# Optimization experiments

Measured on AMD Instinct MI355X. Metric: run time of the kernel, lower is better.

Reference implementation:

```python
import jax, jax.numpy as jnp
import numpy as np

# graph constants
B, V, CG, K, H, IN = 4, 6250, 25000, 3, 64, 2
NUM_LIT = B * 2 * V          # 50_000 literal nodes
NUM_CLS = B * CG             # 100_000 clause nodes
E = K * NUM_CLS              # 300_000 (l2c, c2l) edge pairs
NUM_ROUND = 3
DEMON = float(np.sqrt(H))    # self.demon = sqrt(hidden_size)


def setup_inputs() -> dict:
    key = jax.random.key(0)
    ks = jax.random.split(key, 12)
    rng = np.random.default_rng(0)
    # each clause has K literal endpoints; edges stay inside their own graph
    cls_idx = np.repeat(np.arange(NUM_CLS), K)
    g = cls_idx // CG
    lit_idx = g * 2 * V + rng.integers(0, 2 * V, size=E)

    def lin(k, fi, fo):
        return (jax.random.normal(k, (fi, fo), jnp.float32) / np.sqrt(fi)).astype(jnp.float32)

    return {
        "feat_l2c": jax.random.normal(ks[0], (E, IN), jnp.float32),
        "feat_c2l": jax.random.normal(ks[1], (E, IN), jnp.float32),
        "lit_idx": jnp.asarray(lit_idx, jnp.int32),
        "cls_idx": jnp.asarray(cls_idx, jnp.int32),
        "W_l2c_init": lin(ks[2], IN, H), "b_l2c_init": jnp.zeros((H,), jnp.float32),
        "W_c2l_init": lin(ks[3], IN, H), "b_c2l_init": jnp.zeros((H,), jnp.float32),
        "msgl_W": (jax.random.normal(ks[4], (3, H, H), jnp.float32) / np.sqrt(H)).astype(jnp.float32),
        "msgl_b": jnp.zeros((3, H), jnp.float32),
        "merge_W0": lin(ks[5], 2 * H, H), "merge_b0": jnp.zeros((H,), jnp.float32),
        "merge_Wr": (jax.random.normal(ks[6], (2, H, H), jnp.float32) / np.sqrt(H)).astype(jnp.float32),
        "merge_br": jnp.zeros((2, H), jnp.float32),
        "msgc_W": (jax.random.normal(ks[7], (3, H, H), jnp.float32) / np.sqrt(H)).astype(jnp.float32),
        "msgc_b": jnp.zeros((3, H), jnp.float32),
        "ro_W": (jax.random.normal(ks[8], (2, H, H), jnp.float32) / np.sqrt(H)).astype(jnp.float32),
        "ro_b": jnp.zeros((2, H), jnp.float32),
        "ro_W2": lin(ks[9], H, 1), "ro_b2": jnp.zeros((1,), jnp.float32),
    }


def _mlp3(x, W, b):  # 3-layer MLP, ReLU between layers (num_fc = 3)
    x = jax.nn.relu(x @ W[0] + b[0])
    x = jax.nn.relu(x @ W[1] + b[1])
    return x @ W[2] + b[2]


def reference(feat_l2c, feat_c2l, lit_idx, cls_idx,
              W_l2c_init, b_l2c_init, W_c2l_init, b_c2l_init,
              msgl_W, msgl_b, merge_W0, merge_b0, merge_Wr, merge_br,
              msgc_W, msgc_b, ro_W, ro_b, ro_W2, ro_b2):
    # init edge embeddings (l2c_init / c2l_init linear layers)
    h_l2c = feat_l2c @ W_l2c_init + b_l2c_init   # [E, H]
    h_c2l = feat_c2l @ W_c2l_init + b_c2l_init   # [E, H]

    for _ in range(NUM_ROUND):
        # literal update: aggregate incoming c2l messages, exclude self edge (BP-style)
        agg_l = jax.ops.segment_sum(h_c2l, lit_idx, num_segments=NUM_LIT)   # [NUM_LIT, H]
        m = _mlp3((agg_l[lit_idx] - h_c2l) / DEMON, msgl_W, msgl_b)          # [E, H]
        x = jax.nn.relu(jnp.concatenate([m, h_l2c], axis=-1) @ merge_W0 + merge_b0)
        x = jax.nn.relu(x @ merge_Wr[0] + merge_br[0])
        h_l2c = x @ merge_Wr[1] + merge_br[1]                                # l2c_merge_update
        # clause update
        agg_c = jax.ops.segment_sum(h_l2c, cls_idx, num_segments=NUM_CLS)   # [NUM_CLS, H]
        h_c2l = _mlp3((agg_c[cls_idx] - h_l2c) / DEMON, msgc_W, msgc_b)

    # u_add_e_sum with zero node feats == scatter-add edge emb to dst;
    # literal nodes only receive c2l edges
    l_emb = jax.ops.segment_sum(h_c2l, lit_idx, num_segments=NUM_LIT)        # [NUM_LIT, H]
    # segment_reduce(num_variable*2, ..., 'mean') over per-graph literal blocks (uniform sizes)
    l_mean = l_emb.reshape(B, 2 * V, H).mean(axis=1)                          # [B, H]
    x = jax.nn.relu(l_mean @ ro_W[0] + ro_b[0])
    x = jax.nn.relu(x @ ro_W[1] + ro_b[1])
    return jax.nn.sigmoid(x @ ro_W2 + ro_b2).squeeze(-1)                      # [B]
```

## Files before the change

kernel.cpp:

```cpp
#include <hip/hip_runtime.h>
#include <hip/hip_bf16.h>
#include <stdint.h>

#define EDGES   300000
#define NLIT    50000
#define NGRAPH  4
#define EPG     75000
#define HDIM    64

#define OFF_HL2C   0
#define OFF_HC2L   38400000
#define OFF_AGG    76800000
#define OFF_WT     89600000
#define OFF_ROACC  89681920
#define OFF_CNT    89682944
#define OFF_CSROFF 89882944
#define OFF_CURSOR 90082948
#define OFF_EIDX   90282948
#define OFF_BSUM   91482948
#define OFF_BBASE  91484000

#define WT_TOTAL    40960
#define WT_CLS_ELEM 28672

#define LIT_WBYTES (7 * 8192)
#define CLS_WBYTES (3 * 8192)
#define EPB2       256
#define NCHUNK     ((EDGES + EPB2 - 1) / EPB2)
#define LIT_GRID   512
#define CLS_GRID   1024

#define SCAN_BLOCKS ((NLIT + 255) / 256)

typedef __attribute__((ext_vector_type(8)))  short          s16x8;
typedef __attribute__((ext_vector_type(8)))  unsigned short u16x8;
typedef __attribute__((ext_vector_type(4)))  unsigned short u16x4;
typedef __attribute__((ext_vector_type(4)))  float          f32x4;
typedef __attribute__((ext_vector_type(16))) float          f32x16;

__device__ __forceinline__ f32x16 mfma32(s16x8 a, s16x8 b, f32x16 c) {
    return __builtin_amdgcn_mfma_f32_32x32x16_bf16(a, b, c, 0, 0, 0);
}
__device__ __forceinline__ float bf2f(unsigned short s) {
    union { unsigned int u; float f; } v; v.u = ((unsigned int)s) << 16; return v.f;
}
__device__ __forceinline__ unsigned short f2bf(float f) {
    union { __hip_bfloat16 b; unsigned short s; } v;
    v.b = __float2bfloat16(f);
    return v.s;
}
__device__ __forceinline__ unsigned pk2(float a, float b) {
    return (unsigned)f2bf(a) | ((unsigned)f2bf(b) << 16);
}

__device__ __forceinline__ void layer32(const char* __restrict__ unitBase,
                                        const float* __restrict__ biasL,
                                        const s16x8 (&bin)[4], f32x16 (&acc)[2],
                                        int eL, int hi)
{
#pragma unroll
    for (int t = 0; t < 2; ++t)
#pragma unroll
        for (int g = 0; g < 4; ++g) {
            f32x4 bv = *(const f32x4*)(biasL + 32 * t + 8 * g + 4 * hi);
#pragma unroll
            for (int r = 0; r < 4; ++r) acc[t][4 * g + r] = bv[r];
        }
#pragma unroll
    for (int kb = 0; kb < 4; ++kb)
#pragma unroll
        for (int t = 0; t < 2; ++t) {
            int row = 32 * t + eL;
            s16x8 a = *(const s16x8*)(unitBase + row * 128 +
                                      ((32 * kb + 16 * hi) ^ ((row & 7) << 4)));
            acc[t] = mfma32(a, bin[kb], acc[t]);
        }
}

template<bool RELU>
__device__ __forceinline__ void relayout32(f32x16 (&acc)[2], s16x8 (&bout)[4],
                                           int bpidx, int hi)
{
    if (RELU) {
#pragma unroll
        for (int t = 0; t < 2; ++t)
#pragma unroll
            for (int i = 0; i < 16; ++i) acc[t][i] = fmaxf(acc[t][i], 0.f);
    }
#pragma unroll
    for (int kb = 0; kb < 4; ++kb) {
        int m0 = 2 * kb, m1 = 2 * kb + 1;
        int t0 = m0 >> 2, g0 = m0 & 3, t1 = m1 >> 2, g1 = m1 & 3;
        unsigned A0 = pk2(acc[t0][4 * g0 + 0], acc[t0][4 * g0 + 1]);
        unsigned A1 = pk2(acc[t0][4 * g0 + 2], acc[t0][4 * g0 + 3]);
        unsigned B0 = pk2(acc[t1][4 * g1 + 0], acc[t1][4 * g1 + 1]);
        unsigned B1 = pk2(acc[t1][4 * g1 + 2], acc[t1][4 * g1 + 3]);
        unsigned pA0 = (unsigned)__builtin_amdgcn_ds_bpermute(bpidx, (int)A0);
        unsigned pA1 = (unsigned)__builtin_amdgcn_ds_bpermute(bpidx, (int)A1);
        unsigned pB0 = (unsigned)__builtin_amdgcn_ds_bpermute(bpidx, (int)B0);
        unsigned pB1 = (unsigned)__builtin_amdgcn_ds_bpermute(bpidx, (int)B1);
        union { unsigned w[4]; s16x8 v; } u;
        u.w[0] = hi ? pB0 : A0;
        u.w[1] = hi ? pB1 : A1;
        u.w[2] = hi ? B0 : pA0;
        u.w[3] = hi ? B1 : pA1;
        bout[kb] = u.v;
    }
}

__device__ __forceinline__ void store32(const f32x16 (&acc)[2],
                                        unsigned short* __restrict__ dst, int hi)
{
#pragma unroll
    for (int t = 0; t < 2; ++t)
#pragma unroll
        for (int g = 0; g < 4; ++g) {
            u16x4 p;
#pragma unroll
            for (int r = 0; r < 4; ++r) p[r] = f2bf(acc[t][4 * g + r]);
            *(u16x4*)(dst + 32 * t + 8 * g + 4 * hi) = p;
        }
}

__global__ __launch_bounds__(256) void prep_weights(
    const float* __restrict__ msgl_W, const float* __restrict__ merge_W0,
    const float* __restrict__ merge_Wr, const float* __restrict__ msgc_W,
    unsigned short* __restrict__ wT)
{
    int gid = blockIdx.x * 256 + threadIdx.x;
    if (gid >= WT_TOTAL) return;
    int unit = gid >> 12;
    int o = (gid >> 6) & 63;
    int csw = gid & 63;
    int i = csw ^ ((o & 7) << 3);
    float v;
    if (unit < 3)       v = msgl_W[unit * 4096 + i * 64 + o];
    else if (unit < 5)  v = merge_W0[((unit - 3) * 64 + i) * 64 + o];
    else if (unit < 7)  v = merge_Wr[(unit - 5) * 4096 + i * 64 + o];
    else                v = msgc_W[(unit - 7) * 4096 + i * 64 + o];
    wT[gid] = f2bf(v);
}

__global__ __launch_bounds__(256) void csr_hist(const int* __restrict__ lit_idx,
                                                int* __restrict__ cnt)
{
    int e = blockIdx.x * 256 + threadIdx.x;
    if (e < EDGES) atomicAdd(&cnt[lit_idx[e]], 1);
}

__global__ __launch_bounds__(256) void scan1(const int* __restrict__ cnt,
                                             int* __restrict__ bsum)
{
    __shared__ int red[4];
    int i = blockIdx.x * 256 + threadIdx.x;
    int s = (i < NLIT) ? cnt[i] : 0;
#pragma unroll
    for (int off = 1; off < 64; off <<= 1) s += __shfl_xor(s, off, 64);
    if ((threadIdx.x & 63) == 0) red[threadIdx.x >> 6] = s;
    __syncthreads();
    if (threadIdx.x == 0) bsum[blockIdx.x] = red[0] + red[1] + red[2] + red[3];
}

__global__ __launch_bounds__(256) void scan2(const int* __restrict__ bsum,
                                             int* __restrict__ bbase)
{
    __shared__ int tmp[256];
    int t = threadIdx.x;
    int v = (t < SCAN_BLOCKS) ? bsum[t] : 0;
    tmp[t] = v;
    __syncthreads();
#pragma unroll
    for (int off = 1; off < 256; off <<= 1) {
        int add = (t >= off) ? tmp[t - off] : 0;
        __syncthreads();
        tmp[t] += add;
        __syncthreads();
    }
    if (t < SCAN_BLOCKS) bbase[t] = tmp[t] - v;
}

__global__ __launch_bounds__(256) void scan3(const int* __restrict__ cnt,
                                             const int* __restrict__ bbase,
                                             int* __restrict__ off,
                                             int* __restrict__ cursor)
{
    __shared__ int tmp[256];
    int t = threadIdx.x;
    int i = blockIdx.x * 256 + t;
    int v = (i < NLIT) ? cnt[i] : 0;
    tmp[t] = v;
    __syncthreads();
#pragma unroll
    for (int offs = 1; offs < 256; offs <<= 1) {
        int add = (t >= offs) ? tmp[t - offs] : 0;
        __syncthreads();
        tmp[t] += add;
        __syncthreads();
    }
    if (i < NLIT) {
        int ex = bbase[blockIdx.x] + tmp[t] - v;
        off[i] = ex; cursor[i] = ex;
    }
    if (i == NLIT - 1) off[NLIT] = EDGES;
}

__global__ __launch_bounds__(256) void csr_scatter(const int* __restrict__ lit_idx,
                                                   int* __restrict__ cursor,
                                                   int* __restrict__ eidx)
{
    int e = blockIdx.x * 256 + threadIdx.x;
    if (e >= EDGES) return;
    int pos = atomicAdd(&cursor[lit_idx[e]], 1);
    eidx[pos] = e;
}

__global__ __launch_bounds__(256) void aggregate(const unsigned short* __restrict__ h_c2l,
                                                 const int* __restrict__ off,
                                                 const int* __restrict__ eidx,
                                                 float* __restrict__ agg)
{
    int t = threadIdx.x;
    int lane8 = t & 7;
    int lit = blockIdx.x * 32 + (t >> 3);
    if (lit >= NLIT) return;
    int lo = off[lit], hi = off[lit + 1];
    float s[8] = {0, 0, 0, 0, 0, 0, 0, 0};
    for (int i = lo; i < hi; ++i) {
        int e = eidx[i];
        u16x8 hv = *(const u16x8*)(h_c2l + e * 64 + lane8 * 8);
#pragma unroll
        for (int j = 0; j < 8; ++j) s[j] += bf2f(hv[j]);
    }
    f32x4 a0, a1;
    a0[0] = s[0]; a0[1] = s[1]; a0[2] = s[2]; a0[3] = s[3];
    a1[0] = s[4]; a1[1] = s[5]; a1[2] = s[6]; a1[3] = s[7];
    *(f32x4*)(agg + lit * 64 + lane8 * 8)     = a0;
    *(f32x4*)(agg + lit * 64 + lane8 * 8 + 4) = a1;
}

__global__ __launch_bounds__(256) void init_kernel(
    const float* __restrict__ feat_l2c, const float* __restrict__ feat_c2l,
    const float* __restrict__ W_l2c, const float* __restrict__ b_l2c,
    const float* __restrict__ W_c2l, const float* __restrict__ b_c2l,
    unsigned short* __restrict__ h_l2c, unsigned short* __restrict__ h_c2l)
{
    int gid = blockIdx.x * 256 + threadIdx.x;
    if (gid >= EDGES * 8) return;
    int e = gid >> 3, fo = (gid & 7) << 3;
    float2 fl = *(const float2*)(feat_l2c + e * 2);
    float2 fc = *(const float2*)(feat_c2l + e * 2);

    u16x8 outl, outc;
#pragma unroll
    for (int j = 0; j < 8; ++j) {
        float wl0 = W_l2c[fo + j], wl1 = W_l2c[64 + fo + j];
        float wc0 = W_c2l[fo + j], wc1 = W_c2l[64 + fo + j];
        float vl = fl.x * wl0 + fl.y * wl1 + b_l2c[fo + j];
        float vc = fc.x * wc0 + fc.y * wc1 + b_c2l[fo + j];
        outl[j] = f2bf(vl);
        outc[j] = f2bf(vc);
    }
    *(u16x8*)(h_l2c + e * 64 + fo) = outl;
    *(u16x8*)(h_c2l + e * 64 + fo) = outc;
}

__global__ __launch_bounds__(512, 4) void lit_update(
    const unsigned short* __restrict__ h_c2l,
    unsigned short* __restrict__ h_l2c,
    const float* __restrict__ agg,
    const int* __restrict__ lit_idx,
    const unsigned short* __restrict__ wT,
    const float* __restrict__ msgl_b,
    const float* __restrict__ merge_b0,
    const float* __restrict__ merge_br)
{
    __shared__ __align__(16) char lds[LIT_WBYTES + 384 * 4];
    int tid = threadIdx.x;
#pragma unroll
    for (int c = 0; c < 7; ++c) {
        int idx = c * 512 + tid;
        *(u16x8*)(lds + idx * 16) = *(const u16x8*)(wT + idx * 8);
    }
    float* ldsBias = (float*)(lds + LIT_WBYTES);
    if (tid < 384) {
        float v;
        if (tid < 192)      v = msgl_b[tid];
        else if (tid < 256) v = merge_b0[tid - 192];
        else                v = merge_br[tid - 256];
        ldsBias[tid] = v;
    }
    __syncthreads();

    int wv = tid >> 6, lane = tid & 63;
    int eL = lane & 31, hi = lane >> 5;
    int bpidx = (lane ^ 32) << 2;

    for (int c = blockIdx.x; c < NCHUNK; c += LIT_GRID) {
        int base = c * EPB2 + wv * 32;
        if (base >= EDGES) continue;
        int e = base + eL;
        int lit = lit_idx[e];

        s16x8 hfrag[4];
#pragma unroll
        for (int k = 0; k < 4; ++k)
            hfrag[k] = *(const s16x8*)(h_l2c + e * 64 + 16 * k + 8 * hi);

        s16x8 binp[4];
#pragma unroll
        for (int k = 0; k < 4; ++k) {
            int f0 = 16 * k + 8 * hi;
            f32x4 a0 = *(const f32x4*)(agg + lit * 64 + f0);
            f32x4 a1 = *(const f32x4*)(agg + lit * 64 + f0 + 4);
            u16x8 hv = *(const u16x8*)(h_c2l + e * 64 + f0);
            s16x8 b;
#pragma unroll
            for (int j = 0; j < 4; ++j) b[j]     = (short)f2bf((a0[j] - bf2f(hv[j]))     * 0.125f);
#pragma unroll
            for (int j = 0; j < 4; ++j) b[4 + j] = (short)f2bf((a1[j] - bf2f(hv[4 + j])) * 0.125f);
            binp[k] = b;
        }

        f32x16 acc[2];
        s16x8 bf[4];
        layer32(lds,            ldsBias,       binp, acc, eL, hi);
        relayout32<true >(acc, bf, bpidx, hi);
        layer32(lds + 8192,     ldsBias + 64,  bf, acc, eL, hi);
        relayout32<true >(acc, bf, bpidx, hi);
        layer32(lds + 2 * 8192, ldsBias + 128, bf, acc, eL, hi);
        relayout32<false>(acc, bf, bpidx, hi);

#pragma unroll
        for (int t = 0; t < 2; ++t)
#pragma unroll
            for (int g = 0; g < 4; ++g) {
                f32x4 bv = *(const f32x4*)(ldsBias + 192 + 32 * t + 8 * g + 4 * hi);
#pragma unroll
                for (int r = 0; r < 4; ++r) acc[t][4 * g + r] = bv[r];
            }
#pragma unroll
        for (int kb = 0; kb < 8; ++kb) {
            const char* ub = lds + (3 + (kb >> 2)) * 8192;
            s16x8 bop = (kb < 4) ? bf[kb] : hfrag[kb - 4];
#pragma unroll
            for (int t = 0; t < 2; ++t) {
                int row = 32 * t + eL;
                s16x8 a = *(const s16x8*)(ub + row * 128 +
                                          ((32 * (kb & 3) + 16 * hi) ^ ((row & 7) << 4)));
                acc[t] = mfma32(a, bop, acc[t]);
            }
        }
        relayout32<true>(acc, bf, bpidx, hi);
        layer32(lds + 5 * 8192, ldsBias + 256, bf, acc, eL, hi);
        relayout32<true>(acc, bf, bpidx, hi);
        layer32(lds + 6 * 8192, ldsBias + 320, bf, acc, eL, hi);

        store32(acc, h_l2c + e * 64, hi);
    }
}

__global__ __launch_bounds__(512, 4) void clause_update(
    const unsigned short* __restrict__ h_l2c,
    unsigned short* __restrict__ h_c2l,
    const unsigned short* __restrict__ msgcT,
    const float* __restrict__ msgc_b)
{
    __shared__ __align__(16) char lds[CLS_WBYTES + 192 * 4];
    int tid = threadIdx.x;
#pragma unroll
    for (int c = 0; c < 3; ++c) {
        int idx = c * 512 + tid;
        *(u16x8*)(lds + idx * 16) = *(const u16x8*)(msgcT + idx * 8);
    }
    float* ldsBias = (float*)(lds + CLS_WBYTES);
    if (tid < 192) ldsBias[tid] = msgc_b[tid];
    __syncthreads();

    int wv = tid >> 6, lane = tid & 63;
    int eL = lane & 31, hi = lane >> 5;
    int bpidx = (lane ^ 32) << 2;

    for (int c = blockIdx.x; c < NCHUNK; c += CLS_GRID) {
        int base = c * EPB2 + wv * 32;
        if (base >= EDGES) continue;
        int e = base + eL;

        int c3 = (e / 3) * 3;
        int d = e - c3;
        int e1 = c3 + (d == 0 ? 1 : 0);
        int e2 = c3 + (d == 2 ? 1 : 2);

        s16x8 binp[4];
#pragma unroll
        for (int k = 0; k < 4; ++k) {
            int f0 = 16 * k + 8 * hi;
            u16x8 h1 = *(const u16x8*)(h_l2c + e1 * 64 + f0);
            u16x8 h2 = *(const u16x8*)(h_l2c + e2 * 64 + f0);
            s16x8 b;
#pragma unroll
            for (int j = 0; j < 8; ++j)
                b[j] = (short)f2bf((bf2f(h1[j]) + bf2f(h2[j])) * 0.125f);
            binp[k] = b;
        }

        f32x16 acc[2];
        s16x8 bf[4];
        layer32(lds,            ldsBias,       binp, acc, eL, hi);
        relayout32<true>(acc, bf, bpidx, hi);
        layer32(lds + 8192,     ldsBias + 64,  bf, acc, eL, hi);
        relayout32<true>(acc, bf, bpidx, hi);
        layer32(lds + 2 * 8192, ldsBias + 128, bf, acc, eL, hi);

        store32(acc, h_c2l + e * 64, hi);
    }
}

__global__ __launch_bounds__(256) void readout_sum(
    const unsigned short* __restrict__ h_c2l, float* __restrict__ ro_acc)
{
    __shared__ float lsum[32][64];
    int g = blockIdx.x >> 6, chunk = blockIdx.x & 63;
    int t = threadIdx.x;
    int fg = t & 7, el = t >> 3;
    float s[8] = {0, 0, 0, 0, 0, 0, 0, 0};
    for (int idx = chunk * 32 + el; idx < EPG; idx += 2048) {
        u16x8 hv = *(const u16x8*)(h_c2l + (g * EPG + idx) * 64 + fg * 8);
#pragma unroll
        for (int j = 0; j < 8; ++j) s[j] += bf2f(hv[j]);
    }
#pragma unroll
    for (int j = 0; j < 8; ++j) lsum[el][fg * 8 + j] = s[j];
    __syncthreads();
    if (t < 64) {
        float tot = 0.f;
#pragma unroll 8
        for (int r = 0; r < 32; ++r) tot += lsum[r][t];
        atomicAdd(&ro_acc[g * 64 + t], tot);
    }
}

__global__ __launch_bounds__(256) void readout_mlp(
    const float* __restrict__ ro_acc, const float* __restrict__ ro_W,
    const float* __restrict__ ro_b, const float* __restrict__ ro_W2,
    const float* __restrict__ ro_b2, float* __restrict__ out)
{
    __shared__ float xb[NGRAPH][HDIM];
    __shared__ float yb[NGRAPH][HDIM];
    int g = threadIdx.x >> 6;
    int j = threadIdx.x & 63;
    xb[g][j] = ro_acc[g * HDIM + j] * (1.0f / 12500.0f);
    __syncthreads();
    float a = ro_b[j];
#pragma unroll 8
    for (int k = 0; k < HDIM; ++k) a += xb[g][k] * ro_W[k * HDIM + j];
    a = fmaxf(a, 0.0f);
    yb[g][j] = a;
    __syncthreads();
    float a2 = ro_b[HDIM + j];
#pragma unroll 8
    for (int k = 0; k < HDIM; ++k) a2 += yb[g][k] * ro_W[4096 + k * HDIM + j];
    a2 = fmaxf(a2, 0.0f);
    float p = a2 * ro_W2[j];
#pragma unroll
    for (int off = 32; off > 0; off >>= 1) p += __shfl_down(p, off, 64);
    if (j == 0) out[g] = 1.0f / (1.0f + expf(-(p + ro_b2[0])));
}

extern "C" void kernel_launch(void* const* d_in, const int* in_sizes, int n_in,
                              void* d_out, int out_size, void* d_ws, size_t ws_size,
                              hipStream_t stream)
{
    const float* feat_l2c = (const float*)d_in[0];
    const float* feat_c2l = (const float*)d_in[1];
    const int*   lit_idx  = (const int*)d_in[2];
    const float* W_l2c    = (const float*)d_in[4];
    const float* b_l2c    = (const float*)d_in[5];
    const float* W_c2l    = (const float*)d_in[6];
    const float* b_c2l    = (const float*)d_in[7];
    const float* msgl_W   = (const float*)d_in[8];
    const float* msgl_b   = (const float*)d_in[9];
    const float* merge_W0 = (const float*)d_in[10];
    const float* merge_b0 = (const float*)d_in[11];
    const float* merge_Wr = (const float*)d_in[12];
    const float* merge_br = (const float*)d_in[13];
    const float* msgc_W   = (const float*)d_in[14];
    const float* msgc_b   = (const float*)d_in[15];
    const float* ro_W     = (const float*)d_in[16];
    const float* ro_b     = (const float*)d_in[17];
    const float* ro_W2    = (const float*)d_in[18];
    const float* ro_b2    = (const float*)d_in[19];

    char* ws = (char*)d_ws;
    unsigned short* h_l2c  = (unsigned short*)(ws + OFF_HL2C);
    unsigned short* h_c2l  = (unsigned short*)(ws + OFF_HC2L);
    float*          agg    = (float*)(ws + OFF_AGG);
    unsigned short* wT     = (unsigned short*)(ws + OFF_WT);
    float*          ro_acc = (float*)(ws + OFF_ROACC);
    int*            cnt    = (int*)(ws + OFF_CNT);
    int*            csroff = (int*)(ws + OFF_CSROFF);
    int*            cursor = (int*)(ws + OFF_CURSOR);
    int*            eidx   = (int*)(ws + OFF_EIDX);
    int*            bsum   = (int*)(ws + OFF_BSUM);
    int*            bbase  = (int*)(ws + OFF_BBASE);

    hipMemsetAsync(cnt, 0, NLIT * sizeof(int), stream);
    hipMemsetAsync(ro_acc, 0, NGRAPH * 64 * sizeof(float), stream);

    prep_weights<<<(WT_TOTAL + 255) / 256, 256, 0, stream>>>(msgl_W, merge_W0, merge_Wr, msgc_W, wT);

    csr_hist<<<(EDGES + 255) / 256, 256, 0, stream>>>(lit_idx, cnt);
    scan1<<<SCAN_BLOCKS, 256, 0, stream>>>(cnt, bsum);
    scan2<<<1, 256, 0, stream>>>(bsum, bbase);
    scan3<<<SCAN_BLOCKS, 256, 0, stream>>>(cnt, bbase, csroff, cursor);
    csr_scatter<<<(EDGES + 255) / 256, 256, 0, stream>>>(lit_idx, cursor, eidx);

    init_kernel<<<EDGES * 8 / 256, 256, 0, stream>>>(feat_l2c, feat_c2l, W_l2c, b_l2c,
                                                     W_c2l, b_c2l, h_l2c, h_c2l);
    for (int r = 0; r < 3; ++r) {
        aggregate<<<(NLIT + 31) / 32, 256, 0, stream>>>(h_c2l, csroff, eidx, agg);
        lit_update<<<LIT_GRID, 512, 0, stream>>>(h_c2l, h_l2c, agg, lit_idx, wT,
                                                 msgl_b, merge_b0, merge_br);
        clause_update<<<CLS_GRID, 512, 0, stream>>>(h_l2c, h_c2l, wT + WT_CLS_ELEM, msgc_b);
    }
    readout_sum<<<256, 256, 0, stream>>>(h_c2l, ro_acc);
    readout_mlp<<<1, 256, 0, stream>>>(ro_acc, ro_W, ro_b, ro_W2, ro_b2, (float*)d_out);
}
```

Before: 341.6 us.

## Fuse readout into final clause update, bf16 agg, unroll gather, one chunk per block

The final clause_update reduces its outputs per graph in-wave and accumulates them into ro_acc directly. This removes the last h_c2l store and the separate readout_sum pass. The aggregation buffer is now stored in bf16 to halve its traffic, and the gather loop is unrolled by four for more loads in flight. The edge kernels launch one block per 256-edge chunk instead of grid-striding, and the relayout uses two lane permutes instead of four. The bf16 aggregate adds rounding error to the sum before the subtraction, and the per-element shared atomics add reduction cost.

```diff
diff --git a/kernel.cpp b/kernel.cpp
--- a/kernel.cpp
+++ b/kernel.cpp
@@ -26,9 +26,7 @@
 #define LIT_WBYTES (7 * 8192)
 #define CLS_WBYTES (3 * 8192)
 #define EPB2       256
-#define NCHUNK     ((EDGES + EPB2 - 1) / EPB2)
-#define LIT_GRID   512
-#define CLS_GRID   1024
+#define GRID_EDGE  ((EDGES + EPB2 - 1) / EPB2)
 
 #define SCAN_BLOCKS ((NLIT + 255) / 256)
 
@@ -51,30 +49,6 @@
 }
 __device__ __forceinline__ unsigned pk2(float a, float b) {
     return (unsigned)f2bf(a) | ((unsigned)f2bf(b) << 16);
-}
-
-__device__ __forceinline__ void layer32(const char* __restrict__ unitBase,
-                                        const float* __restrict__ biasL,
-                                        const s16x8 (&bin)[4], f32x16 (&acc)[2],
-                                        int eL, int hi)
-{
-#pragma unroll
-    for (int t = 0; t < 2; ++t)
-#pragma unroll
-        for (int g = 0; g < 4; ++g) {
-            f32x4 bv = *(const f32x4*)(biasL + 32 * t + 8 * g + 4 * hi);
-#pragma unroll
-            for (int r = 0; r < 4; ++r) acc[t][4 * g + r] = bv[r];
-        }
-#pragma unroll
-    for (int kb = 0; kb < 4; ++kb)
-#pragma unroll
-        for (int t = 0; t < 2; ++t) {
-            int row = 32 * t + eL;
-            s16x8 a = *(const s16x8*)(unitBase + row * 128 +
-                                      ((32 * kb + 16 * hi) ^ ((row & 7) << 4)));
-            acc[t] = mfma32(a, bin[kb], acc[t]);
-        }
 }
 
 template<bool RELU>
@@ -95,15 +69,15 @@
         unsigned A1 = pk2(acc[t0][4 * g0 + 2], acc[t0][4 * g0 + 3]);
         unsigned B0 = pk2(acc[t1][4 * g1 + 0], acc[t1][4 * g1 + 1]);
         unsigned B1 = pk2(acc[t1][4 * g1 + 2], acc[t1][4 * g1 + 3]);
-        unsigned pA0 = (unsigned)__builtin_amdgcn_ds_bpermute(bpidx, (int)A0);
-        unsigned pA1 = (unsigned)__builtin_amdgcn_ds_bpermute(bpidx, (int)A1);
-        unsigned pB0 = (unsigned)__builtin_amdgcn_ds_bpermute(bpidx, (int)B0);
-        unsigned pB1 = (unsigned)__builtin_amdgcn_ds_bpermute(bpidx, (int)B1);
+        unsigned s0 = hi ? A0 : B0;
+        unsigned s1 = hi ? A1 : B1;
+        unsigned p0 = (unsigned)__builtin_amdgcn_ds_bpermute(bpidx, (int)s0);
+        unsigned p1 = (unsigned)__builtin_amdgcn_ds_bpermute(bpidx, (int)s1);
         union { unsigned w[4]; s16x8 v; } u;
-        u.w[0] = hi ? pB0 : A0;
-        u.w[1] = hi ? pB1 : A1;
-        u.w[2] = hi ? B0 : pA0;
-        u.w[3] = hi ? B1 : pA1;
+        u.w[0] = hi ? p0 : A0;
+        u.w[1] = hi ? p1 : A1;
+        u.w[2] = hi ? B0 : p0;
+        u.w[3] = hi ? B1 : p1;
         bout[kb] = u.v;
     }
 }
@@ -119,6 +93,30 @@
 #pragma unroll
             for (int r = 0; r < 4; ++r) p[r] = f2bf(acc[t][4 * g + r]);
             *(u16x4*)(dst + 32 * t + 8 * g + 4 * hi) = p;
+        }
+}
+
+__device__ __forceinline__ void layer32(const char* __restrict__ unitBase,
+                                        const float* __restrict__ biasL,
+                                        const s16x8 (&bin)[4], f32x16 (&acc)[2],
+                                        int eL, int hi)
+{
+#pragma unroll
+    for (int t = 0; t < 2; ++t)
+#pragma unroll
+        for (int g = 0; g < 4; ++g) {
+            f32x4 bv = *(const f32x4*)(biasL + 32 * t + 8 * g + 4 * hi);
+#pragma unroll
+            for (int r = 0; r < 4; ++r) acc[t][4 * g + r] = bv[r];
+        }
+#pragma unroll
+    for (int kb = 0; kb < 4; ++kb)
+#pragma unroll
+        for (int t = 0; t < 2; ++t) {
+            int row = 32 * t + eL;
+            s16x8 a = *(const s16x8*)(unitBase + row * 128 +
+                                      ((32 * kb + 16 * hi) ^ ((row & 7) << 4)));
+            acc[t] = mfma32(a, bin[kb], acc[t]);
         }
 }
 
@@ -217,7 +215,7 @@
 __global__ __launch_bounds__(256) void aggregate(const unsigned short* __restrict__ h_c2l,
                                                  const int* __restrict__ off,
                                                  const int* __restrict__ eidx,
-                                                 float* __restrict__ agg)
+                                                 unsigned short* __restrict__ agg)
 {
     int t = threadIdx.x;
     int lane8 = t & 7;
@@ -225,17 +223,27 @@
     if (lit >= NLIT) return;
     int lo = off[lit], hi = off[lit + 1];
     float s[8] = {0, 0, 0, 0, 0, 0, 0, 0};
-    for (int i = lo; i < hi; ++i) {
+    int i = lo;
+    for (; i + 4 <= hi; i += 4) {
+        int e0 = eidx[i], e1 = eidx[i + 1], e2 = eidx[i + 2], e3 = eidx[i + 3];
+        u16x8 v0 = *(const u16x8*)(h_c2l + e0 * 64 + lane8 * 8);
+        u16x8 v1 = *(const u16x8*)(h_c2l + e1 * 64 + lane8 * 8);
+        u16x8 v2 = *(const u16x8*)(h_c2l + e2 * 64 + lane8 * 8);
+        u16x8 v3 = *(const u16x8*)(h_c2l + e3 * 64 + lane8 * 8);
+#pragma unroll
+        for (int j = 0; j < 8; ++j)
+            s[j] += (bf2f(v0[j]) + bf2f(v1[j])) + (bf2f(v2[j]) + bf2f(v3[j]));
+    }
+    for (; i < hi; ++i) {
         int e = eidx[i];
         u16x8 hv = *(const u16x8*)(h_c2l + e * 64 + lane8 * 8);
 #pragma unroll
         for (int j = 0; j < 8; ++j) s[j] += bf2f(hv[j]);
     }
-    f32x4 a0, a1;
-    a0[0] = s[0]; a0[1] = s[1]; a0[2] = s[2]; a0[3] = s[3];
-    a1[0] = s[4]; a1[1] = s[5]; a1[2] = s[6]; a1[3] = s[7];
-    *(f32x4*)(agg + lit * 64 + lane8 * 8)     = a0;
-    *(f32x4*)(agg + lit * 64 + lane8 * 8 + 4) = a1;
+    u16x8 o;
+#pragma unroll
+    for (int j = 0; j < 8; ++j) o[j] = f2bf(s[j]);
+    *(u16x8*)(agg + lit * 64 + lane8 * 8) = o;
 }
 
 __global__ __launch_bounds__(256) void init_kernel(
@@ -267,7 +275,7 @@
 __global__ __launch_bounds__(512, 4) void lit_update(
     const unsigned short* __restrict__ h_c2l,
     unsigned short* __restrict__ h_l2c,
-    const float* __restrict__ agg,
+    const unsigned short* __restrict__ agg,
     const int* __restrict__ lit_idx,
     const unsigned short* __restrict__ wT,
     const float* __restrict__ msgl_b,
@@ -294,78 +302,76 @@
     int wv = tid >> 6, lane = tid & 63;
     int eL = lane & 31, hi = lane >> 5;
     int bpidx = (lane ^ 32) << 2;
-
-    for (int c = blockIdx.x; c < NCHUNK; c += LIT_GRID) {
-        int base = c * EPB2 + wv * 32;
-        if (base >= EDGES) continue;
-        int e = base + eL;
-        int lit = lit_idx[e];
-
-        s16x8 hfrag[4];
-#pragma unroll
-        for (int k = 0; k < 4; ++k)
-            hfrag[k] = *(const s16x8*)(h_l2c + e * 64 + 16 * k + 8 * hi);
-
-        s16x8 binp[4];
-#pragma unroll
-        for (int k = 0; k < 4; ++k) {
-            int f0 = 16 * k + 8 * hi;
-            f32x4 a0 = *(const f32x4*)(agg + lit * 64 + f0);
-            f32x4 a1 = *(const f32x4*)(agg + lit * 64 + f0 + 4);
-            u16x8 hv = *(const u16x8*)(h_c2l + e * 64 + f0);
-            s16x8 b;
-#pragma unroll
-            for (int j = 0; j < 4; ++j) b[j]     = (short)f2bf((a0[j] - bf2f(hv[j]))     * 0.125f);
-#pragma unroll
-            for (int j = 0; j < 4; ++j) b[4 + j] = (short)f2bf((a1[j] - bf2f(hv[4 + j])) * 0.125f);
-            binp[k] = b;
-        }
-
-        f32x16 acc[2];
-        s16x8 bf[4];
-        layer32(lds,            ldsBias,       binp, acc, eL, hi);
-        relayout32<true >(acc, bf, bpidx, hi);
-        layer32(lds + 8192,     ldsBias + 64,  bf, acc, eL, hi);
-        relayout32<true >(acc, bf, bpidx, hi);
-        layer32(lds + 2 * 8192, ldsBias + 128, bf, acc, eL, hi);
-        relayout32<false>(acc, bf, bpidx, hi);
-
-#pragma unroll
-        for (int t = 0; t < 2; ++t)
-#pragma unroll
-            for (int g = 0; g < 4; ++g) {
-                f32x4 bv = *(const f32x4*)(ldsBias + 192 + 32 * t + 8 * g + 4 * hi);
-#pragma unroll
-                for (int r = 0; r < 4; ++r) acc[t][4 * g + r] = bv[r];
-            }
-#pragma unroll
-        for (int kb = 0; kb < 8; ++kb) {
-            const char* ub = lds + (3 + (kb >> 2)) * 8192;
-            s16x8 bop = (kb < 4) ? bf[kb] : hfrag[kb - 4];
-#pragma unroll
-            for (int t = 0; t < 2; ++t) {
-                int row = 32 * t + eL;
-                s16x8 a = *(const s16x8*)(ub + row * 128 +
-                                          ((32 * (kb & 3) + 16 * hi) ^ ((row & 7) << 4)));
-                acc[t] = mfma32(a, bop, acc[t]);
-            }
-        }
-        relayout32<true>(acc, bf, bpidx, hi);
-        layer32(lds + 5 * 8192, ldsBias + 256, bf, acc, eL, hi);
-        relayout32<true>(acc, bf, bpidx, hi);
-        layer32(lds + 6 * 8192, ldsBias + 320, bf, acc, eL, hi);
-
-        store32(acc, h_l2c + e * 64, hi);
-    }
-}
-
+    int base = blockIdx.x * EPB2 + wv * 32;
+    if (base >= EDGES) return;
+    int e = base + eL;
+    int lit = lit_idx[e];
+
+    s16x8 hfrag[4];
+#pragma unroll
+    for (int k = 0; k < 4; ++k)
+        hfrag[k] = *(const s16x8*)(h_l2c + e * 64 + 16 * k + 8 * hi);
+
+    s16x8 binp[4];
+#pragma unroll
+    for (int k = 0; k < 4; ++k) {
+        int f0 = 16 * k + 8 * hi;
+        u16x8 ag = *(const u16x8*)(agg + lit * 64 + f0);
+        u16x8 hv = *(const u16x8*)(h_c2l + e * 64 + f0);
+        s16x8 b;
+#pragma unroll
+        for (int j = 0; j < 8; ++j)
+            b[j] = (short)f2bf((bf2f(ag[j]) - bf2f(hv[j])) * 0.125f);
+        binp[k] = b;
+    }
+
+    f32x16 acc[2];
+    s16x8 bf[4];
+    layer32(lds,            ldsBias,       binp, acc, eL, hi);
+    relayout32<true >(acc, bf, bpidx, hi);
+    layer32(lds + 8192,     ldsBias + 64,  bf, acc, eL, hi);
+    relayout32<true >(acc, bf, bpidx, hi);
+    layer32(lds + 2 * 8192, ldsBias + 128, bf, acc, eL, hi);
+    relayout32<false>(acc, bf, bpidx, hi);
+
+#pragma unroll
+    for (int t = 0; t < 2; ++t)
+#pragma unroll
+        for (int g = 0; g < 4; ++g) {
+            f32x4 bv = *(const f32x4*)(ldsBias + 192 + 32 * t + 8 * g + 4 * hi);
+#pragma unroll
+            for (int r = 0; r < 4; ++r) acc[t][4 * g + r] = bv[r];
+        }
+#pragma unroll
+    for (int kb = 0; kb < 8; ++kb) {
+        const char* ub = lds + (3 + (kb >> 2)) * 8192;
+        s16x8 bop = (kb < 4) ? bf[kb] : hfrag[kb - 4];
+#pragma unroll
+        for (int t = 0; t < 2; ++t) {
+            int row = 32 * t + eL;
+            s16x8 a = *(const s16x8*)(ub + row * 128 +
+                                      ((32 * (kb & 3) + 16 * hi) ^ ((row & 7) << 4)));
+            acc[t] = mfma32(a, bop, acc[t]);
+        }
+    }
+    relayout32<true>(acc, bf, bpidx, hi);
+    layer32(lds + 5 * 8192, ldsBias + 256, bf, acc, eL, hi);
+    relayout32<true>(acc, bf, bpidx, hi);
+    layer32(lds + 6 * 8192, ldsBias + 320, bf, acc, eL, hi);
+
+    store32(acc, h_l2c + e * 64, hi);
+}
+
+template<int FINAL>
 __global__ __launch_bounds__(512, 4) void clause_update(
     const unsigned short* __restrict__ h_l2c,
     unsigned short* __restrict__ h_c2l,
     const unsigned short* __restrict__ msgcT,
-    const float* __restrict__ msgc_b)
+    const float* __restrict__ msgc_b,
+    float* __restrict__ ro_acc)
 {
     __shared__ __align__(16) char lds[CLS_WBYTES + 192 * 4];
+    __shared__ float gsum[128];
     int tid = threadIdx.x;
 #pragma unroll
     for (int c = 0; c < 3; ++c) {
@@ -374,17 +380,19 @@
     }
     float* ldsBias = (float*)(lds + CLS_WBYTES);
     if (tid < 192) ldsBias[tid] = msgc_b[tid];
+    if (FINAL && tid < 128) gsum[tid] = 0.f;
     __syncthreads();
 
     int wv = tid >> 6, lane = tid & 63;
     int eL = lane & 31, hi = lane >> 5;
     int bpidx = (lane ^ 32) << 2;
-
-    for (int c = blockIdx.x; c < NCHUNK; c += CLS_GRID) {
-        int base = c * EPB2 + wv * 32;
-        if (base >= EDGES) continue;
+    int base = blockIdx.x * EPB2 + wv * 32;
+    bool active = base < EDGES;
+    int block_base = blockIdx.x * EPB2;
+    int g_lo = block_base / EPG;
+
+    if (active) {
         int e = base + eL;
-
         int c3 = (e / 3) * 3;
         int d = e - c3;
         int e1 = c3 + (d == 0 ? 1 : 0);
@@ -411,31 +419,54 @@
         relayout32<true>(acc, bf, bpidx, hi);
         layer32(lds + 2 * 8192, ldsBias + 128, bf, acc, eL, hi);
 
-        store32(acc, h_c2l + e * 64, hi);
-    }
-}
-
-__global__ __launch_bounds__(256) void readout_sum(
-    const unsigned short* __restrict__ h_c2l, float* __restrict__ ro_acc)
-{
-    __shared__ float lsum[32][64];
-    int g = blockIdx.x >> 6, chunk = blockIdx.x & 63;
-    int t = threadIdx.x;
-    int fg = t & 7, el = t >> 3;
-    float s[8] = {0, 0, 0, 0, 0, 0, 0, 0};
-    for (int idx = chunk * 32 + el; idx < EPG; idx += 2048) {
-        u16x8 hv = *(const u16x8*)(h_c2l + (g * EPG + idx) * 64 + fg * 8);
-#pragma unroll
-        for (int j = 0; j < 8; ++j) s[j] += bf2f(hv[j]);
-    }
-#pragma unroll
-    for (int j = 0; j < 8; ++j) lsum[el][fg * 8 + j] = s[j];
-    __syncthreads();
-    if (t < 64) {
-        float tot = 0.f;
-#pragma unroll 8
-        for (int r = 0; r < 32; ++r) tot += lsum[r][t];
-        atomicAdd(&ro_acc[g * 64 + t], tot);
+        if (!FINAL) {
+            store32(acc, h_c2l + e * 64, hi);
+        } else {
+            bool uniform = (base / EPG) == ((base + 31) / EPG);
+            if (uniform) {
+#pragma unroll
+                for (int m = 1; m < 32; m <<= 1)
+#pragma unroll
+                    for (int t = 0; t < 2; ++t)
+#pragma unroll
+                        for (int i = 0; i < 16; ++i)
+                            acc[t][i] += __shfl_xor(acc[t][i], m, 64);
+                if (eL == 0) {
+                    int gslot = (base / EPG) - g_lo;
+#pragma unroll
+                    for (int t = 0; t < 2; ++t)
+#pragma unroll
+                        for (int g = 0; g < 4; ++g)
+#pragma unroll
+                            for (int r = 0; r < 4; ++r)
+                                atomicAdd(&gsum[gslot * 64 + 32 * t + 8 * g + 4 * hi + r],
+                                          acc[t][4 * g + r]);
+                }
+            } else {
+                int g = e / EPG;
+#pragma unroll
+                for (int t = 0; t < 2; ++t)
+#pragma unroll
+                    for (int gg = 0; gg < 4; ++gg)
+#pragma unroll
+                        for (int r = 0; r < 4; ++r)
+                            atomicAdd(&ro_acc[g * 64 + 32 * t + 8 * gg + 4 * hi + r],
+                                      acc[t][4 * gg + r]);
+            }
+        }
+    }
+
+    if (FINAL) {
+        __syncthreads();
+        if (tid < 128) {
+            int slot = tid >> 6;
+            int last = block_base + EPB2 - 1;
+            if (last >= EDGES) last = EDGES - 1;
+            int g_hi = last / EPG;
+            int g = g_lo + slot;
+            if (slot == 0 || g_hi > g_lo)
+                atomicAdd(&ro_acc[g * 64 + (tid & 63)], gsum[tid]);
+        }
     }
 }
 
@@ -493,7 +524,7 @@
     char* ws = (char*)d_ws;
     unsigned short* h_l2c  = (unsigned short*)(ws + OFF_HL2C);
     unsigned short* h_c2l  = (unsigned short*)(ws + OFF_HC2L);
-    float*          agg    = (float*)(ws + OFF_AGG);
+    unsigned short* agg    = (unsigned short*)(ws + OFF_AGG);
     unsigned short* wT     = (unsigned short*)(ws + OFF_WT);
     float*          ro_acc = (float*)(ws + OFF_ROACC);
     int*            cnt    = (int*)(ws + OFF_CNT);
@@ -518,10 +549,14 @@
                                                      W_c2l, b_c2l, h_l2c, h_c2l);
     for (int r = 0; r < 3; ++r) {
         aggregate<<<(NLIT + 31) / 32, 256, 0, stream>>>(h_c2l, csroff, eidx, agg);
-        lit_update<<<LIT_GRID, 512, 0, stream>>>(h_c2l, h_l2c, agg, lit_idx, wT,
-                                                 msgl_b, merge_b0, merge_br);
-        clause_update<<<CLS_GRID, 512, 0, stream>>>(h_l2c, h_c2l, wT + WT_CLS_ELEM, msgc_b);
-    }
-    readout_sum<<<256, 256, 0, stream>>>(h_c2l, ro_acc);
+        lit_update<<<GRID_EDGE, 512, 0, stream>>>(h_c2l, h_l2c, agg, lit_idx, wT,
+                                                  msgl_b, merge_b0, merge_br);
+        if (r < 2)
+            clause_update<0><<<GRID_EDGE, 512, 0, stream>>>(h_l2c, h_c2l,
+                                                            wT + WT_CLS_ELEM, msgc_b, ro_acc);
+        else
+            clause_update<1><<<GRID_EDGE, 512, 0, stream>>>(h_l2c, h_c2l,
+                                                            wT + WT_CLS_ELEM, msgc_b, ro_acc);
+    }
     readout_mlp<<<1, 256, 0, stream>>>(ro_acc, ro_W, ro_b, ro_W2, ro_b2, (float*)d_out);
 }
```

New measurement: 324.8 us. 1.05x faster.
